# Optimization experiments

Hardware: AMD Instinct MI355X
Metric: run time of the kernel (lower is better)

Reference implementation:

```python
import jax, jax.numpy as jnp
import numpy as np
import math

# Constants matching init_kwargs
H = 16            # num_attention_heads
K = 8             # tisa_num_kernels
NUM_AGNOSTIC = 2  # num_position_agnostic_heads
MAX_FV = 512.0
MIN_FV = 8.0
P_EPS = 1e-8
EPS = 1e-8


def _slopes():
    # ALiBi-like geometric slope schedule from the module __init__ (non-learned buffer)
    first = -math.log(P_EPS) / (MIN_FV / 2.0)
    last = -math.log(P_EPS) / (MAX_FV / 2.0)
    aware = H - NUM_AGNOSTIC
    s = first * (last / first) ** (jnp.arange(H, dtype=jnp.float32) / (aware - 1))
    # position-agnostic heads get zero slope
    return s * (jnp.arange(H) < aware).astype(jnp.float32)


def setup_inputs() -> dict:
    key = jax.random.key(0)
    ks = jax.random.split(key, 5)
    B, L, D = 4, 1024, 64
    q = jax.random.normal(ks[0], (B, H, L, D), jnp.float32)
    k = jax.random.normal(ks[1], (B, H, L, D), jnp.float32)
    v = jax.random.normal(ks[2], (B, H, L, D), jnp.float32)
    offsets = jax.random.normal(ks[3], (1, K, H, 1, 1), jnp.float32) * 15.0
    amplitudes = jax.random.normal(ks[4], (1, K, H, 1, 1), jnp.float32) * 0.01
    sharpness = jnp.full((1, K, H, 1, 1), 5.0, jnp.float32)
    bias_param = jnp.ones((1, H, 1, 1), jnp.float32)
    return {"q": q, "k": k, "v": v, "offsets": offsets, "amplitudes": amplitudes,
            "sharpness": sharpness, "bias_param": bias_param}


def reference(q, k, v, offsets, amplitudes, sharpness, bias_param):
    B, Hh, L, D = q.shape
    rel = jnp.arange(-L + 1, L, dtype=q.dtype)            # (2L-1,) relative positions
    slopes = _slopes()                                     # (H,)
    exp_decay = -jnp.abs(rel)[None, :] * slopes[:, None]   # (H, 2L-1)

    off = offsets.reshape(K, Hh, 1)
    amp = amplitudes.reshape(K, Hh, 1)
    sh = sharpness.reshape(K, Hh, 1)
    # sigmoid kernel per (kernel, head, relpos); eval mode -> no dropout
    kernel = jnp.abs(amp) * jax.nn.sigmoid(jnp.sign(amp) * ((rel[None, None, :] - off) / sh))
    ksum = kernel.sum(axis=0)                              # (H, 2L-1)
    bias_rel = jnp.log(ksum + EPS + bias_param.reshape(Hh, 1))
    rel_bias = bias_rel + exp_decay                        # (H, 2L-1)

    # relative -> absolute: bias[i, j] = rel_bias[j - i + L - 1]
    idx = jnp.arange(L)[None, :] - jnp.arange(L)[:, None] + (L - 1)  # (L, L)
    attn_bias = rel_bias[:, idx]                           # (H, L, L)

    scale = 1.0 / jnp.sqrt(jnp.asarray(D, q.dtype))
    scores = jnp.einsum('bhqd,bhkd->bhqk', q, k) * scale + attn_bias[None]
    probs = jax.nn.softmax(scores, axis=-1)
    return jnp.einsum('bhqk,bhkd->bhqd', probs, v)
```

## Files before the change

kernel.cpp:

```cpp
#include <hip/hip_runtime.h>
#include <math.h>

#define Bq 4
#define Hh 16
#define Lq 1024
#define Dd 64
#define Kk 8
#define NREL 2047
#define QT 64
#define KT 64
#define SR 72
#define FMAX 8.0f

typedef __attribute__((ext_vector_type(8))) short short8;
typedef __attribute__((ext_vector_type(4))) float f32x4;

__device__ __forceinline__ short f2bf(float x) {
    unsigned u = __float_as_uint(x);
    u += 0x7FFFu + ((u >> 16) & 1u);
    return (short)(u >> 16);
}

__global__ __launch_bounds__(256) void prep_kernel(
    const float* __restrict__ kf, const float* __restrict__ vf,
    const float* __restrict__ off, const float* __restrict__ amp,
    const float* __restrict__ sh, const float* __restrict__ bias_param,
    short* __restrict__ kb, short* __restrict__ vt,
    float* __restrict__ rel_bias)
{
    __shared__ __align__(16) short tile[64 * SR];
    const int blk = blockIdx.x;
    const int t = threadIdx.x;

    if (blk < 2048) {
        int i = blk * 256 + t;
        const float4* s = (const float4*)kf + (size_t)i * 2;
        float4 a = s[0], b = s[1];
        short8 o;
        o[0]=f2bf(a.x); o[1]=f2bf(a.y); o[2]=f2bf(a.z); o[3]=f2bf(a.w);
        o[4]=f2bf(b.x); o[5]=f2bf(b.y); o[6]=f2bf(b.z); o[7]=f2bf(b.w);
        *((short8*)kb + i) = o;
    } else if (blk < 3072) {
        int m = blk - 2048;
        int jt = m & 15, bh = m >> 4;
        const float* base = vf + ((size_t)bh * Lq + jt * 64) * Dd;
        #pragma unroll
        for (int c = 0; c < 4; ++c) {
            int fi = c * 256 + t;
            int row = fi >> 4, col = (fi & 15) * 4;
            float4 a = *(const float4*)(base + row * Dd + col);
            short* p = &tile[row * SR + col];
            p[0]=f2bf(a.x); p[1]=f2bf(a.y); p[2]=f2bf(a.z); p[3]=f2bf(a.w);
        }
        __syncthreads();
        int d = t >> 2, js = (t & 3) * 16;
        __align__(16) short buf[16];
        #pragma unroll
        for (int u = 0; u < 16; ++u) buf[u] = tile[(js + u) * SR + d];
        short* dst = vt + ((size_t)bh * Dd + d) * Lq + jt * 64 + js;
        *(short8*)dst       = *(short8*)&buf[0];
        *(short8*)(dst + 8) = *(short8*)&buf[8];
    } else {
        int idx = (blk - 3072) * 256 + t;
        if (idx >= Hh * NREL) return;
        int h = idx / NREL;
        int r = idx % NREL;
        float rel = (float)(r - (Lq - 1));
        const float first = 4.605170185988092f;
        float slope = 0.0f;
        if (h < Hh - 2) slope = first * powf(1.0f / 64.0f, (float)h / 13.0f);
        float exp_decay = -fabsf(rel) * slope;
        float ksum = 0.0f;
        #pragma unroll
        for (int kk = 0; kk < Kk; ++kk) {
            float a = amp[kk * Hh + h];
            float o = off[kk * Hh + h];
            float s = sh[kk * Hh + h];
            float sgn = (a > 0.0f) ? 1.0f : ((a < 0.0f) ? -1.0f : 0.0f);
            float x = sgn * (rel - o) / s;
            float sig = 1.0f / (1.0f + expf(-x));
            ksum += fabsf(a) * sig;
        }
        rel_bias[idx] = logf(ksum + 1e-8f + bias_param[h]) + exp_decay;
    }
}

__global__ __launch_bounds__(256) void attn_kernel(
    const float* __restrict__ qp, const short* __restrict__ kb,
    const short* __restrict__ vtp, const float* __restrict__ rel_bias,
    float* __restrict__ out)
{
    __shared__ __align__(16) short qp_s[QT * SR];
    __shared__ __align__(16) short k_s[KT * SR];
    __shared__ __align__(16) short v_s[KT * SR];
    __shared__ float bias_s[128];

    const int bh  = blockIdx.x;
    const int qs  = blockIdx.y * QT;
    const int t   = threadIdx.x;
    const int w   = t >> 6;
    const int lane = t & 63;
    const int quad = lane >> 4;
    const int l15  = lane & 15;

    const float* qbase = qp + ((size_t)bh * Lq + qs) * Dd;
    #pragma unroll
    for (int c = 0; c < 4; ++c) {
        int fi = c * 256 + t;
        int row = fi >> 4, col = (fi & 15) * 4;
        float4 a = *(const float4*)(qbase + row * Dd + col);
        short* p = &qp_s[row * SR + col];
        p[0]=f2bf(a.x); p[1]=f2bf(a.y); p[2]=f2bf(a.z); p[3]=f2bf(a.w);
    }
    __syncthreads();

    short8 aq0 = *(const short8*)&qp_s[(16 * w + l15) * SR +  0 + quad * 8];
    short8 aq1 = *(const short8*)&qp_s[(16 * w + l15) * SR + 32 + quad * 8];

    const short* ktile = kb  + (size_t)bh * Lq * Dd;
    const short* vtb   = vtp + (size_t)bh * Dd * Lq;
    const float* biash = rel_bias + (size_t)(bh & 15) * NREL;

    f32x4 Of[4];
    float l_part[4];
    #pragma unroll
    for (int nf = 0; nf < 4; ++nf) Of[nf] = (f32x4){0.f, 0.f, 0.f, 0.f};
    #pragma unroll
    for (int r = 0; r < 4; ++r) l_part[r] = 0.f;

    const int ibase = 16 * w + quad * 4;

    for (int kt = 0; kt < Lq / KT; ++kt) {
        const int ks = kt * KT;
        __syncthreads();

        const short* ksrc = ktile + (size_t)ks * Dd;
        #pragma unroll
        for (int p = 0; p < 2; ++p) {
            int idx = p * 256 + t;
            int row = idx >> 3, seg = idx & 7;
            *(short8*)&k_s[row * SR + seg * 8] = *(const short8*)(ksrc + idx * 8);
        }
        #pragma unroll
        for (int p = 0; p < 2; ++p) {
            int idx = p * 256 + t;
            int row = idx >> 3, seg = idx & 7;
            *(short8*)&v_s[row * SR + seg * 8] =
                *(const short8*)(vtb + (size_t)row * Lq + ks + seg * 8);
        }
        if (t < 127) bias_s[t] = biash[ks - qs + 960 + t];
        __syncthreads();

        f32x4 Sf[4];
        #pragma unroll
        for (int nf = 0; nf < 4; ++nf) {
            f32x4 acc = (f32x4){0.f, 0.f, 0.f, 0.f};
            short8 b0 = *(const short8*)&k_s[(nf * 16 + l15) * SR +  0 + quad * 8];
            short8 b1 = *(const short8*)&k_s[(nf * 16 + l15) * SR + 32 + quad * 8];
            acc = __builtin_amdgcn_mfma_f32_16x16x32_bf16(aq0, b0, acc, 0, 0, 0);
            acc = __builtin_amdgcn_mfma_f32_16x16x32_bf16(aq1, b1, acc, 0, 0, 0);
            Sf[nf] = acc;
        }

        #pragma unroll
        for (int r = 0; r < 4; ++r) {
            int irow = ibase + r;
            float su = 0.f;
            #pragma unroll
            for (int nf = 0; nf < 4; ++nf) {
                float s = Sf[nf][r] * 0.125f + bias_s[nf * 16 + l15 - irow + 63];
                float pv = __expf(s - FMAX);
                su += pv;
                qp_s[irow * SR + nf * 16 + l15] = f2bf(pv);
            }
            l_part[r] += su;
        }

        short8 ap0 = *(const short8*)&qp_s[(16 * w + l15) * SR +  0 + quad * 8];
        short8 ap1 = *(const short8*)&qp_s[(16 * w + l15) * SR + 32 + quad * 8];
        #pragma unroll
        for (int nf = 0; nf < 4; ++nf) {
            f32x4 acc = Of[nf];
            short8 b0 = *(const short8*)&v_s[(nf * 16 + l15) * SR +  0 + quad * 8];
            short8 b1 = *(const short8*)&v_s[(nf * 16 + l15) * SR + 32 + quad * 8];
            acc = __builtin_amdgcn_mfma_f32_16x16x32_bf16(ap0, b0, acc, 0, 0, 0);
            acc = __builtin_amdgcn_mfma_f32_16x16x32_bf16(ap1, b1, acc, 0, 0, 0);
            Of[nf] = acc;
        }
    }

    float inv[4];
    #pragma unroll
    for (int r = 0; r < 4; ++r) {
        float l = l_part[r];
        l += __shfl_xor(l, 1);
        l += __shfl_xor(l, 2);
        l += __shfl_xor(l, 4);
        l += __shfl_xor(l, 8);
        inv[r] = 1.f / l;
    }
    float* obase = out + ((size_t)bh * Lq + qs) * Dd;
    #pragma unroll
    for (int nf = 0; nf < 4; ++nf)
        #pragma unroll
        for (int r = 0; r < 4; ++r)
            obase[(size_t)(ibase + r) * Dd + nf * 16 + l15] = Of[nf][r] * inv[r];
}

extern "C" void kernel_launch(void* const* d_in, const int* in_sizes, int n_in,
                              void* d_out, int out_size, void* d_ws, size_t ws_size,
                              hipStream_t stream) {
    const float* q   = (const float*)d_in[0];
    const float* k   = (const float*)d_in[1];
    const float* v   = (const float*)d_in[2];
    const float* off = (const float*)d_in[3];
    const float* amp = (const float*)d_in[4];
    const float* sh  = (const float*)d_in[5];
    const float* bp  = (const float*)d_in[6];
    float* out = (float*)d_out;

    char* ws = (char*)d_ws;
    float* rel_bias = (float*)ws;
    short* kb       = (short*)(ws + 131072);
    short* vt       = (short*)(ws + 131072 + 8388608);

    prep_kernel<<<3200, 256, 0, stream>>>(k, v, off, amp, sh, bp, kb, vt, rel_bias);

    dim3 grid(Bq * Hh, Lq / QT);
    attn_kernel<<<grid, 256, 0, stream>>>(q, kb, vt, rel_bias, out);
}
```

Baseline: 142.3 us.

## Rewrite attention with 32x32 MFMA tiles, register-fed K/V and in-kernel bias

The attention kernel now uses a 128-row query tile with 32x32x16 bf16 MFMAs. K and V fragments are loaded straight from global memory into registers, which removes the shared-memory staging and the block-wide barriers. V is pre-transposed into 64x64 tiles so those loads are contiguous. The relative-position bias is computed per block into shared memory instead of in a separate prep pass, and the softmax scale and log2e are folded into Q and the bias so exp2 can be used. The trade-offs are that every wave re-reads the full K/V tiles from cache, register pressure is higher, and the grid has half as many blocks.

```diff
diff --git a/kernel.cpp b/kernel.cpp
--- a/kernel.cpp
+++ b/kernel.cpp
@@ -6,14 +6,15 @@
 #define Lq 1024
 #define Dd 64
 #define Kk 8
-#define NREL 2047
-#define QT 64
+#define QT 128
 #define KT 64
 #define SR 72
 #define FMAX 8.0f
-
-typedef __attribute__((ext_vector_type(8))) short short8;
-typedef __attribute__((ext_vector_type(4))) float f32x4;
+#define LOG2E 1.44269504f
+
+typedef __attribute__((ext_vector_type(8)))  short short8;
+typedef __attribute__((ext_vector_type(4)))  float f32x4;
+typedef __attribute__((ext_vector_type(16))) float f32x16;
 
 __device__ __forceinline__ short f2bf(float x) {
     unsigned u = __float_as_uint(x);
@@ -23,10 +24,7 @@
 
 __global__ __launch_bounds__(256) void prep_kernel(
     const float* __restrict__ kf, const float* __restrict__ vf,
-    const float* __restrict__ off, const float* __restrict__ amp,
-    const float* __restrict__ sh, const float* __restrict__ bias_param,
-    short* __restrict__ kb, short* __restrict__ vt,
-    float* __restrict__ rel_bias)
+    short* __restrict__ kb, short* __restrict__ vt)
 {
     __shared__ __align__(16) short tile[64 * SR];
     const int blk = blockIdx.x;
@@ -40,7 +38,7 @@
         o[0]=f2bf(a.x); o[1]=f2bf(a.y); o[2]=f2bf(a.z); o[3]=f2bf(a.w);
         o[4]=f2bf(b.x); o[5]=f2bf(b.y); o[6]=f2bf(b.z); o[7]=f2bf(b.w);
         *((short8*)kb + i) = o;
-    } else if (blk < 3072) {
+    } else {
         int m = blk - 2048;
         int jt = m & 15, bh = m >> 4;
         const float* base = vf + ((size_t)bh * Lq + jt * 64) * Dd;
@@ -57,154 +55,141 @@
         __align__(16) short buf[16];
         #pragma unroll
         for (int u = 0; u < 16; ++u) buf[u] = tile[(js + u) * SR + d];
-        short* dst = vt + ((size_t)bh * Dd + d) * Lq + jt * 64 + js;
+        short* dst = vt + (((size_t)(bh * 16 + jt) * 64 + d) * 64) + js;
         *(short8*)dst       = *(short8*)&buf[0];
         *(short8*)(dst + 8) = *(short8*)&buf[8];
-    } else {
-        int idx = (blk - 3072) * 256 + t;
-        if (idx >= Hh * NREL) return;
-        int h = idx / NREL;
-        int r = idx % NREL;
-        float rel = (float)(r - (Lq - 1));
-        const float first = 4.605170185988092f;
-        float slope = 0.0f;
-        if (h < Hh - 2) slope = first * powf(1.0f / 64.0f, (float)h / 13.0f);
-        float exp_decay = -fabsf(rel) * slope;
-        float ksum = 0.0f;
-        #pragma unroll
-        for (int kk = 0; kk < Kk; ++kk) {
-            float a = amp[kk * Hh + h];
-            float o = off[kk * Hh + h];
-            float s = sh[kk * Hh + h];
-            float sgn = (a > 0.0f) ? 1.0f : ((a < 0.0f) ? -1.0f : 0.0f);
-            float x = sgn * (rel - o) / s;
-            float sig = 1.0f / (1.0f + expf(-x));
-            ksum += fabsf(a) * sig;
-        }
-        rel_bias[idx] = logf(ksum + 1e-8f + bias_param[h]) + exp_decay;
     }
 }
 
 __global__ __launch_bounds__(256) void attn_kernel(
-    const float* __restrict__ qp, const short* __restrict__ kb,
-    const short* __restrict__ vtp, const float* __restrict__ rel_bias,
+    const float* __restrict__ qp, const short* __restrict__ kbp,
+    const short* __restrict__ vtp,
+    const float* __restrict__ off, const float* __restrict__ amp,
+    const float* __restrict__ sh, const float* __restrict__ bp,
     float* __restrict__ out)
 {
-    __shared__ __align__(16) short qp_s[QT * SR];
-    __shared__ __align__(16) short k_s[KT * SR];
-    __shared__ __align__(16) short v_s[KT * SR];
-    __shared__ float bias_s[128];
-
-    const int bh  = blockIdx.x;
-    const int qs  = blockIdx.y * QT;
-    const int t   = threadIdx.x;
-    const int w   = t >> 6;
+    __shared__ __align__(16) short p_s[QT * SR];
+    __shared__ float bias_s[1152];
+
+    const int bh = blockIdx.x;
+    const int qs = blockIdx.y * QT;
+    const int t  = threadIdx.x;
+    const int w  = t >> 6;
     const int lane = t & 63;
-    const int quad = lane >> 4;
-    const int l15  = lane & 15;
-
-    const float* qbase = qp + ((size_t)bh * Lq + qs) * Dd;
-    #pragma unroll
-    for (int c = 0; c < 4; ++c) {
-        int fi = c * 256 + t;
-        int row = fi >> 4, col = (fi & 15) * 4;
-        float4 a = *(const float4*)(qbase + row * Dd + col);
-        short* p = &qp_s[row * SR + col];
-        p[0]=f2bf(a.x); p[1]=f2bf(a.y); p[2]=f2bf(a.z); p[3]=f2bf(a.w);
+    const int l31 = lane & 31;
+    const int h5  = lane >> 5;
+    const int h   = bh & 15;
+
+    float slope = (h < Hh - 2) ? 4.605170185988092f * exp2f(-6.0f * (float)h / 13.0f) : 0.0f;
+    #pragma unroll
+    for (int it = 0; it < 5; ++it) {
+        int i = it * 256 + t;
+        if (i < 1151) {
+            float rel = (float)(i - 127 - qs);
+            float ksum = 0.0f;
+            #pragma unroll
+            for (int kk = 0; kk < Kk; ++kk) {
+                float a = amp[kk * Hh + h];
+                float o = off[kk * Hh + h];
+                float s = sh[kk * Hh + h];
+                float sgn = (a > 0.0f) ? 1.0f : ((a < 0.0f) ? -1.0f : 0.0f);
+                float x = sgn * (rel - o) / s;
+                ksum += fabsf(a) / (1.0f + __expf(-x));
+            }
+            bias_s[i] = (logf(ksum + 1e-8f + bp[h]) - fabsf(rel) * slope - FMAX) * LOG2E;
+        }
+    }
+
+    const float QS = 0.125f * LOG2E;
+    short8 aq[4];
+    const float* qrow = qp + ((size_t)bh * Lq + qs + 32 * w + l31) * Dd;
+    #pragma unroll
+    for (int kseg = 0; kseg < 4; ++kseg) {
+        float4 x0 = *(const float4*)(qrow + kseg * 16 + h5 * 8);
+        float4 x1 = *(const float4*)(qrow + kseg * 16 + h5 * 8 + 4);
+        short8 a;
+        a[0]=f2bf(x0.x*QS); a[1]=f2bf(x0.y*QS); a[2]=f2bf(x0.z*QS); a[3]=f2bf(x0.w*QS);
+        a[4]=f2bf(x1.x*QS); a[5]=f2bf(x1.y*QS); a[6]=f2bf(x1.z*QS); a[7]=f2bf(x1.w*QS);
+        aq[kseg] = a;
     }
     __syncthreads();
 
-    short8 aq0 = *(const short8*)&qp_s[(16 * w + l15) * SR +  0 + quad * 8];
-    short8 aq1 = *(const short8*)&qp_s[(16 * w + l15) * SR + 32 + quad * 8];
-
-    const short* ktile = kb  + (size_t)bh * Lq * Dd;
-    const short* vtb   = vtp + (size_t)bh * Dd * Lq;
-    const float* biash = rel_bias + (size_t)(bh & 15) * NREL;
-
-    f32x4 Of[4];
-    float l_part[4];
-    #pragma unroll
-    for (int nf = 0; nf < 4; ++nf) Of[nf] = (f32x4){0.f, 0.f, 0.f, 0.f};
-    #pragma unroll
-    for (int r = 0; r < 4; ++r) l_part[r] = 0.f;
-
-    const int ibase = 16 * w + quad * 4;
-
+    const short* kbb = kbp + (size_t)bh * Lq * Dd;
+    const short* vtb = vtp + (size_t)bh * 16 * 64 * 64;
+
+    f32x16 O0, O1;
+    float l_part[16];
+    #pragma unroll
+    for (int r = 0; r < 16; ++r) { O0[r] = 0.f; O1[r] = 0.f; l_part[r] = 0.f; }
+
+    #pragma unroll 1
     for (int kt = 0; kt < Lq / KT; ++kt) {
         const int ks = kt * KT;
-        __syncthreads();
-
-        const short* ksrc = ktile + (size_t)ks * Dd;
-        #pragma unroll
-        for (int p = 0; p < 2; ++p) {
-            int idx = p * 256 + t;
-            int row = idx >> 3, seg = idx & 7;
-            *(short8*)&k_s[row * SR + seg * 8] = *(const short8*)(ksrc + idx * 8);
-        }
-        #pragma unroll
-        for (int p = 0; p < 2; ++p) {
-            int idx = p * 256 + t;
-            int row = idx >> 3, seg = idx & 7;
-            *(short8*)&v_s[row * SR + seg * 8] =
-                *(const short8*)(vtb + (size_t)row * Lq + ks + seg * 8);
-        }
-        if (t < 127) bias_s[t] = biash[ks - qs + 960 + t];
-        __syncthreads();
-
-        f32x4 Sf[4];
-        #pragma unroll
-        for (int nf = 0; nf < 4; ++nf) {
-            f32x4 acc = (f32x4){0.f, 0.f, 0.f, 0.f};
-            short8 b0 = *(const short8*)&k_s[(nf * 16 + l15) * SR +  0 + quad * 8];
-            short8 b1 = *(const short8*)&k_s[(nf * 16 + l15) * SR + 32 + quad * 8];
-            acc = __builtin_amdgcn_mfma_f32_16x16x32_bf16(aq0, b0, acc, 0, 0, 0);
-            acc = __builtin_amdgcn_mfma_f32_16x16x32_bf16(aq1, b1, acc, 0, 0, 0);
-            Sf[nf] = acc;
-        }
-
-        #pragma unroll
-        for (int r = 0; r < 4; ++r) {
-            int irow = ibase + r;
-            float su = 0.f;
-            #pragma unroll
-            for (int nf = 0; nf < 4; ++nf) {
-                float s = Sf[nf][r] * 0.125f + bias_s[nf * 16 + l15 - irow + 63];
-                float pv = __expf(s - FMAX);
-                su += pv;
-                qp_s[irow * SR + nf * 16 + l15] = f2bf(pv);
-            }
-            l_part[r] += su;
-        }
-
-        short8 ap0 = *(const short8*)&qp_s[(16 * w + l15) * SR +  0 + quad * 8];
-        short8 ap1 = *(const short8*)&qp_s[(16 * w + l15) * SR + 32 + quad * 8];
-        #pragma unroll
-        for (int nf = 0; nf < 4; ++nf) {
-            f32x4 acc = Of[nf];
-            short8 b0 = *(const short8*)&v_s[(nf * 16 + l15) * SR +  0 + quad * 8];
-            short8 b1 = *(const short8*)&v_s[(nf * 16 + l15) * SR + 32 + quad * 8];
-            acc = __builtin_amdgcn_mfma_f32_16x16x32_bf16(ap0, b0, acc, 0, 0, 0);
-            acc = __builtin_amdgcn_mfma_f32_16x16x32_bf16(ap1, b1, acc, 0, 0, 0);
-            Of[nf] = acc;
-        }
-    }
-
-    float inv[4];
-    #pragma unroll
-    for (int r = 0; r < 4; ++r) {
+
+        short8 bk0[4], bk1[4];
+        #pragma unroll
+        for (int kseg = 0; kseg < 4; ++kseg) {
+            bk0[kseg] = *(const short8*)(kbb + (size_t)(ks + l31)      * Dd + kseg * 16 + h5 * 8);
+            bk1[kseg] = *(const short8*)(kbb + (size_t)(ks + 32 + l31) * Dd + kseg * 16 + h5 * 8);
+        }
+
+        f32x16 S0, S1;
+        #pragma unroll
+        for (int r = 0; r < 16; ++r) { S0[r] = 0.f; S1[r] = 0.f; }
+        #pragma unroll
+        for (int kseg = 0; kseg < 4; ++kseg) {
+            S0 = __builtin_amdgcn_mfma_f32_32x32x16_bf16(aq[kseg], bk0[kseg], S0, 0, 0, 0);
+            S1 = __builtin_amdgcn_mfma_f32_32x32x16_bf16(aq[kseg], bk1[kseg], S1, 0, 0, 0);
+        }
+
+        const short* vtile = vtb + (size_t)kt * 64 * 64;
+        short8 bv0[4], bv1[4];
+        #pragma unroll
+        for (int kseg = 0; kseg < 4; ++kseg) {
+            bv0[kseg] = *(const short8*)(vtile + (size_t)(l31)      * 64 + kseg * 16 + h5 * 8);
+            bv1[kseg] = *(const short8*)(vtile + (size_t)(32 + l31) * 64 + kseg * 16 + h5 * 8);
+        }
+
+        #pragma unroll
+        for (int r = 0; r < 16; ++r) {
+            int rowpat = (r & 3) + 8 * (r >> 2) + 4 * h5;
+            int irow = 32 * w + rowpat;
+            float b0 = bias_s[ks + l31 - irow + 127];
+            float b1 = bias_s[ks + 32 + l31 - irow + 127];
+            float e0 = __builtin_amdgcn_exp2f(S0[r] + b0);
+            float e1 = __builtin_amdgcn_exp2f(S1[r] + b1);
+            l_part[r] += e0 + e1;
+            p_s[irow * SR + l31]      = f2bf(e0);
+            p_s[irow * SR + 32 + l31] = f2bf(e1);
+        }
+
+        short8 ap[4];
+        #pragma unroll
+        for (int kseg = 0; kseg < 4; ++kseg)
+            ap[kseg] = *(const short8*)&p_s[(32 * w + l31) * SR + kseg * 16 + h5 * 8];
+
+        #pragma unroll
+        for (int kseg = 0; kseg < 4; ++kseg) {
+            O0 = __builtin_amdgcn_mfma_f32_32x32x16_bf16(ap[kseg], bv0[kseg], O0, 0, 0, 0);
+            O1 = __builtin_amdgcn_mfma_f32_32x32x16_bf16(ap[kseg], bv1[kseg], O1, 0, 0, 0);
+        }
+    }
+
+    float* ob = out + ((size_t)bh * Lq + qs) * Dd;
+    #pragma unroll
+    for (int r = 0; r < 16; ++r) {
         float l = l_part[r];
         l += __shfl_xor(l, 1);
         l += __shfl_xor(l, 2);
         l += __shfl_xor(l, 4);
         l += __shfl_xor(l, 8);
-        inv[r] = 1.f / l;
-    }
-    float* obase = out + ((size_t)bh * Lq + qs) * Dd;
-    #pragma unroll
-    for (int nf = 0; nf < 4; ++nf)
-        #pragma unroll
-        for (int r = 0; r < 4; ++r)
-            obase[(size_t)(ibase + r) * Dd + nf * 16 + l15] = Of[nf][r] * inv[r];
+        l += __shfl_xor(l, 16);
+        float inv = 1.0f / l;
+        int rowpat = (r & 3) + 8 * (r >> 2) + 4 * h5;
+        int irow = 32 * w + rowpat;
+        ob[(size_t)irow * Dd + l31]      = O0[r] * inv;
+        ob[(size_t)irow * Dd + 32 + l31] = O1[r] * inv;
+    }
 }
 
 extern "C" void kernel_launch(void* const* d_in, const int* in_sizes, int n_in,
@@ -220,12 +205,11 @@
     float* out = (float*)d_out;
 
     char* ws = (char*)d_ws;
-    float* rel_bias = (float*)ws;
-    short* kb       = (short*)(ws + 131072);
-    short* vt       = (short*)(ws + 131072 + 8388608);
-
-    prep_kernel<<<3200, 256, 0, stream>>>(k, v, off, amp, sh, bp, kb, vt, rel_bias);
+    short* kb = (short*)ws;
+    short* vt = (short*)(ws + 8388608);
+
+    prep_kernel<<<3072, 256, 0, stream>>>(k, v, kb, vt);
 
     dim3 grid(Bq * Hh, Lq / QT);
-    attn_kernel<<<grid, 256, 0, stream>>>(q, kb, vt, rel_bias, out);
-}
+    attn_kernel<<<grid, 256, 0, stream>>>(q, kb, vt, off, amp, sh, bp, out);
+}
```

Measured after the change: 167.8 us. +17.9%, slower.
